# Kernel optimization log

Measured on AMD Instinct MI355X. Metric: run time of the kernel, lower is better.

The kernel has to match this reference:

```python
import jax, jax.numpy as jnp
import numpy as np


def _quantize(mat):
    # per-row (last-dim) symmetric int8 quantization; scale stored in fp16 like torch
    max_val = (jnp.max(jnp.abs(mat), axis=-1) / 127.0).astype(jnp.float16)
    # torch's .to(int8) truncates toward zero; jnp astype does the same for in-range values
    q = (mat / max_val[..., None].astype(mat.dtype)).astype(jnp.int8)
    return q, max_val


def setup_inputs() -> dict:
    key = jax.random.key(0)
    k1, k2, k3, k4 = jax.random.split(key, 4)
    B, S, D_IN, D_OUT = 4, 2048, 4096, 4096
    x = jax.random.normal(k1, (B, S, D_IN), dtype=jnp.float32)
    origin_weight = jax.random.normal(k2, (D_OUT, D_IN), dtype=jnp.float32) * 0.02
    bias = jax.random.normal(k3, (D_OUT,), dtype=jnp.float32) * 0.01
    act_max = jax.random.normal(k4, (D_IN,), dtype=jnp.float32)
    return {"x": x, "origin_weight": origin_weight, "bias": bias,
            "act_max": act_max, "alpha": 32}


def reference(x, origin_weight, bias, act_max, alpha):
    d_in = act_max.shape[-1]
    # get_unq_idx_topk: top-alpha outlier channels by |act_max|
    _, idx = jax.lax.top_k(jnp.abs(act_max), alpha)          # [alpha]
    t = jnp.ones((d_in,), dtype=origin_weight.dtype).at[idx].set(0)

    # weight decomposition + quantization (done in __init__ in torch)
    weight_q, w_max = _quantize(origin_weight * t)           # [out,in] int8, [out] fp16
    weight_unq = origin_weight[:, idx].T                      # [alpha, out]

    # activation decomposition + per-token quantization
    x_unq = x[..., idx]                                       # [B,S,alpha]
    x_q, x_max = _quantize(x * t.astype(x.dtype))             # [B,S,in] int8, [B,S] fp16

    # simulated MatMulInteger: int8 values multiplied in fp32
    res_q = jnp.matmul(x_q.astype(jnp.float32), weight_q.T.astype(jnp.float32))  # [B,S,out]
    mx = (x_max[..., None] * w_max[None, :]).astype(jnp.float32)                  # [B,S,out]
    res_q = (res_q * mx).astype(x.dtype)

    # fp outlier path
    res_unq = jnp.matmul(x_unq, weight_unq) + bias
    return res_q + res_unq
```

## Files before the change

### kernel.cpp

```cpp
#include <hip/hip_runtime.h>
#include <hip/hip_fp16.h>

typedef __attribute__((ext_vector_type(4)))  int   i32x4;
typedef __attribute__((ext_vector_type(16))) int   i32x16;

#define ALPHA 32
#define BM 256
#define BN 128
#define BK 64


__global__ __launch_bounds__(256) void topk_kernel(const float* __restrict__ act_max,
                                                   int* __restrict__ idx_out,
                                                   unsigned* __restrict__ tbits,
                                                   int K) {
  __shared__ float v[4096];
  __shared__ float rv[4];
  __shared__ int   ri[4];
  __shared__ unsigned bits[128];
  const int t = threadIdx.x;
  for (int i = t; i < K; i += 256) v[i] = fabsf(act_max[i]);
  for (int i = t; i < K / 32; i += 256) bits[i] = 0xFFFFFFFFu;
  __syncthreads();
  for (int sel = 0; sel < ALPHA; ++sel) {
    float bv = -1.f; int bi = 0;
    for (int i = t; i < K; i += 256) {
      float x = v[i];
      if (x > bv) { bv = x; bi = i; }
    }
    for (int m = 1; m < 64; m <<= 1) {
      float ov = __shfl_xor(bv, m);
      int   oi = __shfl_xor(bi, m);
      if (ov > bv || (ov == bv && oi < bi)) { bv = ov; bi = oi; }
    }
    if ((t & 63) == 0) { rv[t >> 6] = bv; ri[t >> 6] = bi; }
    __syncthreads();
    if (t == 0) {
      for (int u = 1; u < 4; ++u)
        if (rv[u] > bv || (rv[u] == bv && ri[u] < bi)) { bv = rv[u]; bi = ri[u]; }
      idx_out[sel] = bi;
      v[bi] = -2.f;
      bits[bi >> 5] &= ~(1u << (bi & 31));
    }
    __syncthreads();
  }
  for (int i = t; i < K / 32; i += 256) tbits[i] = bits[i];
}

__global__ __launch_bounds__(256) void quant8_kernel(
    const float* __restrict__ srcW, const float* __restrict__ srcX,
    const unsigned* __restrict__ tbits, const int* __restrict__ idxg,
    signed char* __restrict__ wq, signed char* __restrict__ xq,
    _Float16* __restrict__ wmax, _Float16* __restrict__ xmax,
    float* __restrict__ wuf, float* __restrict__ xuf,
    int nbw, int K, int N, int M) {
  const int t = threadIdx.x, lane = t & 63, w = t >> 6;
  const int b = blockIdx.x;
  const float* src; signed char* q; _Float16* smax; float* unq; int r0, R;
  if (b < nbw) { src = srcW; q = wq; smax = wmax; unq = wuf; r0 = b * 8; R = N; }
  else         { src = srcX; q = xq; smax = xmax; unq = xuf; r0 = (b - nbw) * 8; R = M; }
  __shared__ unsigned bits[128];
  __shared__ signed char qt[8 * 4096];
  for (int i = t; i < 128; i += 256) bits[i] = tbits[i];
  __syncthreads();
  const int shft = (lane & 7) * 4;
#pragma unroll
  for (int g = 0; g < 2; ++g) {
    const int rl = w + 4 * g;
    const float4* srow = (const float4*)(src + (size_t)(r0 + rl) * K);
    float4 v[16];
    float am = 0.f;
#pragma unroll
    for (int j = 0; j < 16; ++j) {
      float4 x = srow[j * 64 + lane];
      unsigned b4 = bits[j * 8 + (lane >> 3)] >> shft;
      if (!(b4 & 1u)) x.x = 0.f;
      if (!(b4 & 2u)) x.y = 0.f;
      if (!(b4 & 4u)) x.z = 0.f;
      if (!(b4 & 8u)) x.w = 0.f;
      v[j] = x;
      am = fmaxf(am, fmaxf(fmaxf(fabsf(x.x), fabsf(x.y)), fmaxf(fabsf(x.z), fabsf(x.w))));
    }
#pragma unroll
    for (int m = 1; m < 64; m <<= 1) am = fmaxf(am, __shfl_xor(am, m));
    const _Float16 sh = (_Float16)(am / 127.0f);
    const float s = (float)sh;
    if (lane == 0) smax[r0 + rl] = sh;
    signed char* row = qt + rl * 4096;
#pragma unroll
    for (int j = 0; j < 16; ++j) {
      float4 x = v[j];
      char4 c;
      c.x = (signed char)(x.x / s);
      c.y = (signed char)(x.y / s);
      c.z = (signed char)(x.z / s);
      c.w = (signed char)(x.w / s);
      const int c2 = j * 16 + (lane >> 2);
      *(char4*)(row + ((c2 ^ rl) << 4) + (lane & 3) * 4) = c;
    }
  }
  __syncthreads();
  const size_t pbase = (size_t)(r0 >> 5) * 32 * K + (size_t)(r0 & 31) * 16;
#pragma unroll
  for (int i = 0; i < 8; ++i) {
    const int s2 = i * 256 + t;
    const int c2 = s2 >> 3, rl = s2 & 7;
    int4 d = *(const int4*)(qt + rl * 4096 + ((c2 ^ rl) << 4));
    *(int4*)(q + pbase + (size_t)c2 * 512 + rl * 16) = d;
  }
  {
    const int j = t >> 3, rl = t & 7;
    unq[(size_t)j * R + r0 + rl] = src[(size_t)(r0 + rl) * K + idxg[j]];
  }
}

__device__ __forceinline__ void gld_lds16(const signed char* g, signed char* l) {
  __builtin_amdgcn_global_load_lds(
      (const __attribute__((address_space(1))) void*)g,
      (__attribute__((address_space(3))) void*)l, 16, 0, 0);
}

__global__ __launch_bounds__(256, 2) void gemm_kernel(
    const signed char* __restrict__ xq, const signed char* __restrict__ wq,
    const _Float16* __restrict__ xmax, const _Float16* __restrict__ wmax,
    const float* __restrict__ xuf,
    const float* __restrict__ wuf,
    const float* __restrict__ bias,
    float* __restrict__ out, int M, int N, int K) {
  __shared__ union {
    struct { signed char A[3][BM * BK]; signed char B[3][BN * BK]; } g;
    struct { float xu[ALPHA * BM]; float wu[ALPHA * BN]; } e;
  } sm;
  __shared__ _Float16 xmh[BM];
  __shared__ _Float16 wmh[BN];
  __shared__ float    bl[BN];

  const int t = threadIdx.x;
  const int bid = blockIdx.y * gridDim.x + blockIdx.x;
  const int xcd = bid & 7, loc = bid >> 3;
  const int bxi = xcd * 4 + (loc & 3);
  const int byi = loc >> 2;
  const int bm0 = byi * BM;
  const int bn0 = bxi * BN;
  const int lane = t & 63, w = t >> 6;
  const int wm = w >> 1, wn = w & 1;
  const int hi = lane >> 5, l31 = lane & 31;

  i32x16 acc[4][2] = {};

  const int tp = t >> 7;
  const int to = (t & 127) * 16;
  const signed char* aS = xq + (size_t)bm0 * K + (size_t)tp * 32 * K + to;
  const signed char* bS = wq + (size_t)bn0 * K + (size_t)tp * 32 * K + to;
  signed char* const aD = &sm.g.A[0][0] + t * 16;
  signed char* const bD = &sm.g.B[0][0] + t * 16;
  const size_t PSTR = (size_t)64 * K;

  auto STAGE = [&](int buf, int kt) {
    const size_t ko = (size_t)kt * 2048;
#pragma unroll
    for (int i = 0; i < 4; ++i)
      gld_lds16(aS + (size_t)i * PSTR + ko, aD + buf * (BM * BK) + i * 4096);
#pragma unroll
    for (int i = 0; i < 2; ++i)
      gld_lds16(bS + (size_t)i * PSTR + ko, bD + buf * (BN * BK) + i * 4096);
  };

  const int NT = K >> 6;
  STAGE(0, 0);
  STAGE(1, 1);
  const signed char* const aR0 = &sm.g.A[0][0] + (wm * 4) * 2048 + 16 * lane;
  const signed char* const bR0 = &sm.g.B[0][0] + (wn * 2) * 2048 + 16 * lane;

  int cur = 0, st = 2;
  for (int kt = 0; kt < NT - 1; ++kt) {
    asm volatile("s_waitcnt vmcnt(6)" ::: "memory");
    asm volatile("s_barrier" ::: "memory");
    const signed char* aRd = aR0 + cur * (BM * BK);
    const signed char* bRd = bR0 + cur * (BN * BK);
    i32x4 af[2][4], bf[2][2];
#pragma unroll
    for (int ks = 0; ks < 2; ++ks) {
#pragma unroll
      for (int mi = 0; mi < 4; ++mi) af[ks][mi] = *(const i32x4*)(aRd + mi * 2048 + ks * 1024);
#pragma unroll
      for (int ni = 0; ni < 2; ++ni) bf[ks][ni] = *(const i32x4*)(bRd + ni * 2048 + ks * 1024);
    }
    if (kt + 2 < NT) STAGE(st, kt + 2);
    __builtin_amdgcn_s_setprio(1);
#pragma unroll
    for (int ks = 0; ks < 2; ++ks)
#pragma unroll
      for (int mi = 0; mi < 4; ++mi)
#pragma unroll
        for (int ni = 0; ni < 2; ++ni)
          acc[mi][ni] = __builtin_amdgcn_mfma_i32_32x32x32_i8(af[ks][mi], bf[ks][ni], acc[mi][ni], 0, 0, 0);
    __builtin_amdgcn_s_setprio(0);
    if (++cur == 3) cur = 0;
    if (++st == 3) st = 0;
  }
  {
    asm volatile("s_waitcnt vmcnt(0)" ::: "memory");
    asm volatile("s_barrier" ::: "memory");
    const signed char* aRd = aR0 + cur * (BM * BK);
    const signed char* bRd = bR0 + cur * (BN * BK);
    i32x4 af[2][4], bf[2][2];
#pragma unroll
    for (int ks = 0; ks < 2; ++ks) {
#pragma unroll
      for (int mi = 0; mi < 4; ++mi) af[ks][mi] = *(const i32x4*)(aRd + mi * 2048 + ks * 1024);
#pragma unroll
      for (int ni = 0; ni < 2; ++ni) bf[ks][ni] = *(const i32x4*)(bRd + ni * 2048 + ks * 1024);
    }
    __builtin_amdgcn_s_setprio(1);
#pragma unroll
    for (int ks = 0; ks < 2; ++ks)
#pragma unroll
      for (int mi = 0; mi < 4; ++mi)
#pragma unroll
        for (int ni = 0; ni < 2; ++ni)
          acc[mi][ni] = __builtin_amdgcn_mfma_i32_32x32x32_i8(af[ks][mi], bf[ks][ni], acc[mi][ni], 0, 0, 0);
    __builtin_amdgcn_s_setprio(0);
  }

  __syncthreads();
  {
    const float4* xs = (const float4*)xuf;
    float4* xl = (float4*)sm.e.xu;
#pragma unroll
    for (int i = 0; i < 8; ++i) {
      int p = i * 256 + t;
      int j = p >> 6, r4 = p & 63;
      xl[p] = xs[(size_t)j * (M >> 2) + (bm0 >> 2) + r4];
    }
    const float4* wsrc = (const float4*)wuf;
    float4* wl = (float4*)sm.e.wu;
#pragma unroll
    for (int i = 0; i < 4; ++i) {
      int p = i * 256 + t;
      int j = p >> 5, r4 = p & 31;
      wl[p] = wsrc[(size_t)j * (N >> 2) + (bn0 >> 2) + r4];
    }
    if (t < BM / 2) ((unsigned*)xmh)[t] = ((const unsigned*)(xmax + bm0))[t];
    if (t < BN / 2) ((unsigned*)wmh)[t] = ((const unsigned*)(wmax + bn0))[t];
    if (t < BN / 4) ((float4*)bl)[t] = ((const float4*)(bias + bn0))[t];
  }
  __syncthreads();

  const int c0 = wn * 64 + l31;
  const _Float16 wh0 = wmh[c0], wh1 = wmh[c0 + 32];
  const float bv0 = bl[c0], bv1 = bl[c0 + 32];
  const float* xul = sm.e.xu;
  const float* wul = sm.e.wu;

#pragma unroll
  for (int mi = 0; mi < 4; ++mi) {
    const int rbase = wm * 128 + mi * 32 + 4 * hi;
    float f0[16], f1[16];
#pragma unroll
    for (int r = 0; r < 16; ++r) {
      int row = rbase + (r & 3) + 8 * (r >> 2);
      _Float16 xh = xmh[row];
      float mx0 = (float)(_Float16)(xh * wh0);
      float mx1 = (float)(_Float16)(xh * wh1);
      f0[r] = (float)acc[mi][0][r] * mx0 + bv0;
      f1[r] = (float)acc[mi][1][r] * mx1 + bv1;
    }
#pragma unroll 4
    for (int j = 0; j < ALPHA; ++j) {
      const float4* xrow4 = (const float4*)(xul + j * BM + rbase);
      float wv0 = wul[j * BN + c0];
      float wv1 = wul[j * BN + c0 + 32];
#pragma unroll
      for (int gq = 0; gq < 4; ++gq) {
        float4 xv = xrow4[gq * 2];
        f0[gq * 4 + 0] += xv.x * wv0;  f1[gq * 4 + 0] += xv.x * wv1;
        f0[gq * 4 + 1] += xv.y * wv0;  f1[gq * 4 + 1] += xv.y * wv1;
        f0[gq * 4 + 2] += xv.z * wv0;  f1[gq * 4 + 2] += xv.z * wv1;
        f0[gq * 4 + 3] += xv.w * wv0;  f1[gq * 4 + 3] += xv.w * wv1;
      }
    }
#pragma unroll
    for (int r = 0; r < 16; ++r) {
      int row = bm0 + rbase + (r & 3) + 8 * (r >> 2);
      size_t o = (size_t)row * N + bn0;
      out[o + c0] = f0[r];
      out[o + c0 + 32] = f1[r];
    }
  }
}

extern "C" void kernel_launch(void* const* d_in, const int* in_sizes, int n_in,
                              void* d_out, int out_size, void* d_ws, size_t ws_size,
                              hipStream_t stream) {
  const float* x       = (const float*)d_in[0];
  const float* W       = (const float*)d_in[1];
  const float* bias    = (const float*)d_in[2];
  const float* act_max = (const float*)d_in[3];
  const int K = in_sizes[3];
  const int N = in_sizes[1] / K;
  const int M = in_sizes[0] / K;
  float* out = (float*)d_out;

  char* ws = (char*)d_ws;
  size_t off = 0;
  auto take = [&](size_t b) { char* p = ws + off; off += (b + 255) & ~(size_t)255; return p; };
  signed char* wq  = (signed char*)take((size_t)N * K);
  signed char* xq  = (signed char*)take((size_t)M * K);
  _Float16* wmax   = (_Float16*)take((size_t)N * 2);
  _Float16* xmax   = (_Float16*)take((size_t)M * 2);
  float* wuf       = (float*)take((size_t)ALPHA * N * 4);
  float* xuf       = (float*)take((size_t)ALPHA * M * 4);
  int* idx         = (int*)take(ALPHA * 4);
  unsigned* tbits  = (unsigned*)take((size_t)(K / 32) * 4);

  const int nbw = N / 8, nbx = M / 8;
  topk_kernel<<<1, 256, 0, stream>>>(act_max, idx, tbits, K);
  quant8_kernel<<<nbw + nbx, 256, 0, stream>>>(W, x, tbits, idx, wq, xq,
                                               wmax, xmax, wuf, xuf, nbw, K, N, M);
  dim3 grid(N / BN, M / BM);
  gemm_kernel<<<grid, 256, 0, stream>>>(xq, wq, xmax, wmax, xuf, wuf, bias, out, M, N, K);
}
```

Before: 276.8 us.

## Enlarge GEMM tile to 256x256 with 8 waves and 4-stage split-phase pipeline

Doubles the N tile to 256 and launches 512-thread blocks (8 waves in a 2x4 arrangement), so each loaded A/B byte is reused across more MFMAs. The k-loop becomes a 4-deep LDS ring with A and B prefetches issued in separate half-iterations, interleaved with barriers, explicit lgkm/vm waits and setprio around MFMA groups. Epilogue scale, bias and outlier staging move into the shared union, and the XCD block remap is adjusted to the new grid. This raises LDS use to 128 KB per block and adds barriers, which may limit occupancy and add synchronisation overhead.

```diff
diff --git a/kernel.cpp b/kernel.cpp
--- a/kernel.cpp
+++ b/kernel.cpp
@@ -6,7 +6,7 @@
 
 #define ALPHA 32
 #define BM 256
-#define BN 128
+#define BN 256
 #define BK 64
 
 
@@ -120,7 +120,7 @@
       (__attribute__((address_space(3))) void*)l, 16, 0, 0);
 }
 
-__global__ __launch_bounds__(256, 2) void gemm_kernel(
+__global__ __launch_bounds__(512, 2) void gemm_kernel(
     const signed char* __restrict__ xq, const signed char* __restrict__ wq,
     const _Float16* __restrict__ xmax, const _Float16* __restrict__ wmax,
     const float* __restrict__ xuf,
@@ -128,108 +128,115 @@
     const float* __restrict__ bias,
     float* __restrict__ out, int M, int N, int K) {
   __shared__ union {
-    struct { signed char A[3][BM * BK]; signed char B[3][BN * BK]; } g;
-    struct { float xu[ALPHA * BM]; float wu[ALPHA * BN]; } e;
+    struct { signed char A[4][BM * BK]; signed char B[4][BN * BK]; } g;
+    struct { float xu[ALPHA * BM]; float wu[ALPHA * BN];
+             _Float16 xmh[BM]; _Float16 wmh[BN]; float bl[BN]; } e;
   } sm;
-  __shared__ _Float16 xmh[BM];
-  __shared__ _Float16 wmh[BN];
-  __shared__ float    bl[BN];
 
   const int t = threadIdx.x;
   const int bid = blockIdx.y * gridDim.x + blockIdx.x;
   const int xcd = bid & 7, loc = bid >> 3;
-  const int bxi = xcd * 4 + (loc & 3);
-  const int byi = loc >> 2;
+  const int bxi = xcd * 2 + (loc & 1);
+  const int byi = loc >> 1;
   const int bm0 = byi * BM;
   const int bn0 = bxi * BN;
   const int lane = t & 63, w = t >> 6;
-  const int wm = w >> 1, wn = w & 1;
+  const int wm = w >> 2, wn = w & 3;
   const int hi = lane >> 5, l31 = lane & 31;
 
   i32x16 acc[4][2] = {};
 
-  const int tp = t >> 7;
-  const int to = (t & 127) * 16;
-  const signed char* aS = xq + (size_t)bm0 * K + (size_t)tp * 32 * K + to;
-  const signed char* bS = wq + (size_t)bn0 * K + (size_t)tp * 32 * K + to;
+  const size_t P32 = (size_t)32 * K;
+  const signed char* aS = xq + (size_t)bm0 * K + (size_t)(t >> 7) * P32 + (t & 127) * 16;
+  const signed char* bS = wq + (size_t)bn0 * K + (size_t)(t >> 7) * P32 + (t & 127) * 16;
   signed char* const aD = &sm.g.A[0][0] + t * 16;
   signed char* const bD = &sm.g.B[0][0] + t * 16;
-  const size_t PSTR = (size_t)64 * K;
-
-  auto STAGE = [&](int buf, int kt) {
+
+  auto STAGE_A = [&](int buf, int kt) {
     const size_t ko = (size_t)kt * 2048;
-#pragma unroll
-    for (int i = 0; i < 4; ++i)
-      gld_lds16(aS + (size_t)i * PSTR + ko, aD + buf * (BM * BK) + i * 4096);
-#pragma unroll
-    for (int i = 0; i < 2; ++i)
-      gld_lds16(bS + (size_t)i * PSTR + ko, bD + buf * (BN * BK) + i * 4096);
+    gld_lds16(aS + ko, aD + buf * (BM * BK));
+    gld_lds16(aS + ko + 4 * P32, aD + buf * (BM * BK) + 8192);
   };
+  auto STAGE_B = [&](int buf, int kt) {
+    const size_t ko = (size_t)kt * 2048;
+    gld_lds16(bS + ko, bD + buf * (BN * BK));
+    gld_lds16(bS + ko + 4 * P32, bD + buf * (BN * BK) + 8192);
+  };
 
   const int NT = K >> 6;
-  STAGE(0, 0);
-  STAGE(1, 1);
-  const signed char* const aR0 = &sm.g.A[0][0] + (wm * 4) * 2048 + 16 * lane;
-  const signed char* const bR0 = &sm.g.B[0][0] + (wn * 2) * 2048 + 16 * lane;
-
-  int cur = 0, st = 2;
-  for (int kt = 0; kt < NT - 1; ++kt) {
-    asm volatile("s_waitcnt vmcnt(6)" ::: "memory");
-    asm volatile("s_barrier" ::: "memory");
-    const signed char* aRd = aR0 + cur * (BM * BK);
-    const signed char* bRd = bR0 + cur * (BN * BK);
-    i32x4 af[2][4], bf[2][2];
-#pragma unroll
-    for (int ks = 0; ks < 2; ++ks) {
-#pragma unroll
-      for (int mi = 0; mi < 4; ++mi) af[ks][mi] = *(const i32x4*)(aRd + mi * 2048 + ks * 1024);
-#pragma unroll
-      for (int ni = 0; ni < 2; ++ni) bf[ks][ni] = *(const i32x4*)(bRd + ni * 2048 + ks * 1024);
-    }
-    if (kt + 2 < NT) STAGE(st, kt + 2);
-    __builtin_amdgcn_s_setprio(1);
-#pragma unroll
-    for (int ks = 0; ks < 2; ++ks)
-#pragma unroll
-      for (int mi = 0; mi < 4; ++mi)
-#pragma unroll
-        for (int ni = 0; ni < 2; ++ni)
-          acc[mi][ni] = __builtin_amdgcn_mfma_i32_32x32x32_i8(af[ks][mi], bf[ks][ni], acc[mi][ni], 0, 0, 0);
-    __builtin_amdgcn_s_setprio(0);
-    if (++cur == 3) cur = 0;
-    if (++st == 3) st = 0;
-  }
-  {
-    asm volatile("s_waitcnt vmcnt(0)" ::: "memory");
-    asm volatile("s_barrier" ::: "memory");
-    const signed char* aRd = aR0 + cur * (BM * BK);
-    const signed char* bRd = bR0 + cur * (BN * BK);
-    i32x4 af[2][4], bf[2][2];
-#pragma unroll
-    for (int ks = 0; ks < 2; ++ks) {
-#pragma unroll
-      for (int mi = 0; mi < 4; ++mi) af[ks][mi] = *(const i32x4*)(aRd + mi * 2048 + ks * 1024);
-#pragma unroll
-      for (int ni = 0; ni < 2; ++ni) bf[ks][ni] = *(const i32x4*)(bRd + ni * 2048 + ks * 1024);
-    }
-    __builtin_amdgcn_s_setprio(1);
-#pragma unroll
-    for (int ks = 0; ks < 2; ++ks)
-#pragma unroll
-      for (int mi = 0; mi < 4; ++mi)
-#pragma unroll
-        for (int ni = 0; ni < 2; ++ni)
-          acc[mi][ni] = __builtin_amdgcn_mfma_i32_32x32x32_i8(af[ks][mi], bf[ks][ni], acc[mi][ni], 0, 0, 0);
-    __builtin_amdgcn_s_setprio(0);
-  }
+  STAGE_A(0, 0); STAGE_B(0, 0);
+  STAGE_A(1, 1); STAGE_B(1, 1);
+  STAGE_A(2, 2); STAGE_B(2, 2);
+  asm volatile("s_waitcnt vmcnt(8)" ::: "memory");
+  asm volatile("s_barrier" ::: "memory");
+
+  const signed char* const aBase = &sm.g.A[0][0] + (wm * 4) * 2048 + hi * 512 + l31 * 16;
+  const signed char* const bBase = &sm.g.B[0][0] + (wn * 2) * 2048 + hi * 512 + l31 * 16;
+
+#define MFMA8()                                                                        \
+  acc[0][0] = __builtin_amdgcn_mfma_i32_32x32x32_i8(a0, b0, acc[0][0], 0, 0, 0);       \
+  acc[0][1] = __builtin_amdgcn_mfma_i32_32x32x32_i8(a0, b1, acc[0][1], 0, 0, 0);       \
+  acc[1][0] = __builtin_amdgcn_mfma_i32_32x32x32_i8(a1, b0, acc[1][0], 0, 0, 0);       \
+  acc[1][1] = __builtin_amdgcn_mfma_i32_32x32x32_i8(a1, b1, acc[1][1], 0, 0, 0);       \
+  acc[2][0] = __builtin_amdgcn_mfma_i32_32x32x32_i8(a2, b0, acc[2][0], 0, 0, 0);       \
+  acc[2][1] = __builtin_amdgcn_mfma_i32_32x32x32_i8(a2, b1, acc[2][1], 0, 0, 0);       \
+  acc[3][0] = __builtin_amdgcn_mfma_i32_32x32x32_i8(a3, b0, acc[3][0], 0, 0, 0);       \
+  acc[3][1] = __builtin_amdgcn_mfma_i32_32x32x32_i8(a3, b1, acc[3][1], 0, 0, 0)
+
+#define ITERATION(DOSTAGE, WSTR)                                                       \
+  {                                                                                    \
+    const signed char* aRd = aBase + cur * (BM * BK);                                  \
+    const signed char* bRd = bBase + cur * (BN * BK);                                  \
+                                                       \
+    i32x4 a0 = *(const i32x4*)(aRd + 0);                                               \
+    i32x4 a1 = *(const i32x4*)(aRd + 2048);                                            \
+    i32x4 a2 = *(const i32x4*)(aRd + 4096);                                            \
+    i32x4 a3 = *(const i32x4*)(aRd + 6144);                                            \
+    i32x4 b0 = *(const i32x4*)(bRd + 0);                                               \
+    i32x4 b1 = *(const i32x4*)(bRd + 2048);                                            \
+    if (DOSTAGE) STAGE_A((kt + 3) & 3, kt + 3);                                        \
+    asm volatile("s_barrier" ::: "memory");                                            \
+    asm volatile("s_waitcnt lgkmcnt(0)" ::: "memory");                                 \
+    __builtin_amdgcn_sched_barrier(0);                                                 \
+    __builtin_amdgcn_s_setprio(1);                                                     \
+    MFMA8();                                                                           \
+    __builtin_amdgcn_s_setprio(0);                                                     \
+    asm volatile("s_barrier" ::: "memory");                                            \
+                                                       \
+    a0 = *(const i32x4*)(aRd + 1024);                                                  \
+    a1 = *(const i32x4*)(aRd + 3072);                                                  \
+    a2 = *(const i32x4*)(aRd + 5120);                                                  \
+    a3 = *(const i32x4*)(aRd + 7168);                                                  \
+    b0 = *(const i32x4*)(bRd + 1024);                                                  \
+    b1 = *(const i32x4*)(bRd + 3072);                                                  \
+    if (DOSTAGE) STAGE_B((kt + 3) & 3, kt + 3);                                        \
+    asm volatile(WSTR ::: "memory");                                                   \
+    asm volatile("s_barrier" ::: "memory");                                            \
+    asm volatile("s_waitcnt lgkmcnt(0)" ::: "memory");                                 \
+    __builtin_amdgcn_sched_barrier(0);                                                 \
+    __builtin_amdgcn_s_setprio(1);                                                     \
+    MFMA8();                                                                           \
+    __builtin_amdgcn_s_setprio(0);                                                     \
+    asm volatile("s_barrier" ::: "memory");                                            \
+    cur = (cur + 1) & 3;                                                               \
+  }
+
+  int cur = 0;
+  int kt = 0;
+  for (; kt < NT - 3; ++kt) ITERATION(true, "s_waitcnt vmcnt(8)");
+  ITERATION(false, "s_waitcnt vmcnt(4)"); ++kt;
+  ITERATION(false, "s_waitcnt vmcnt(0)"); ++kt;
+  ITERATION(false, "s_waitcnt vmcnt(0)");
+#undef ITERATION
+#undef MFMA8
 
   __syncthreads();
   {
     const float4* xs = (const float4*)xuf;
     float4* xl = (float4*)sm.e.xu;
 #pragma unroll
-    for (int i = 0; i < 8; ++i) {
-      int p = i * 256 + t;
+    for (int i = 0; i < 4; ++i) {
+      int p = i * 512 + t;
       int j = p >> 6, r4 = p & 63;
       xl[p] = xs[(size_t)j * (M >> 2) + (bm0 >> 2) + r4];
     }
@@ -237,19 +244,19 @@
     float4* wl = (float4*)sm.e.wu;
 #pragma unroll
     for (int i = 0; i < 4; ++i) {
-      int p = i * 256 + t;
-      int j = p >> 5, r4 = p & 31;
+      int p = i * 512 + t;
+      int j = p >> 6, r4 = p & 63;
       wl[p] = wsrc[(size_t)j * (N >> 2) + (bn0 >> 2) + r4];
     }
-    if (t < BM / 2) ((unsigned*)xmh)[t] = ((const unsigned*)(xmax + bm0))[t];
-    if (t < BN / 2) ((unsigned*)wmh)[t] = ((const unsigned*)(wmax + bn0))[t];
-    if (t < BN / 4) ((float4*)bl)[t] = ((const float4*)(bias + bn0))[t];
+    if (t < BM / 2) ((unsigned*)sm.e.xmh)[t] = ((const unsigned*)(xmax + bm0))[t];
+    if (t < BN / 2) ((unsigned*)sm.e.wmh)[t] = ((const unsigned*)(wmax + bn0))[t];
+    if (t < BN / 4) ((float4*)sm.e.bl)[t] = ((const float4*)(bias + bn0))[t];
   }
   __syncthreads();
 
   const int c0 = wn * 64 + l31;
-  const _Float16 wh0 = wmh[c0], wh1 = wmh[c0 + 32];
-  const float bv0 = bl[c0], bv1 = bl[c0 + 32];
+  const _Float16 wh0 = sm.e.wmh[c0], wh1 = sm.e.wmh[c0 + 32];
+  const float bv0 = sm.e.bl[c0], bv1 = sm.e.bl[c0 + 32];
   const float* xul = sm.e.xu;
   const float* wul = sm.e.wu;
 
@@ -260,7 +267,7 @@
 #pragma unroll
     for (int r = 0; r < 16; ++r) {
       int row = rbase + (r & 3) + 8 * (r >> 2);
-      _Float16 xh = xmh[row];
+      _Float16 xh = sm.e.xmh[row];
       float mx0 = (float)(_Float16)(xh * wh0);
       float mx1 = (float)(_Float16)(xh * wh1);
       f0[r] = (float)acc[mi][0][r] * mx0 + bv0;
@@ -319,5 +326,5 @@
   quant8_kernel<<<nbw + nbx, 256, 0, stream>>>(W, x, tbits, idx, wq, xq,
                                                wmax, xmax, wuf, xuf, nbw, K, N, M);
   dim3 grid(N / BN, M / BM);
-  gemm_kernel<<<grid, 256, 0, stream>>>(xq, wq, xmax, wmax, xuf, wuf, bias, out, M, N, K);
-}
+  gemm_kernel<<<grid, 512, 0, stream>>>(xq, wq, xmax, wmax, xuf, wuf, bias, out, M, N, K);
+}
```

New measurement: 272.9 us. No clear change (-1.4%).

## Load GEMM B operand straight into registers and use a 4-deep LDS ring for A

Applied to the files above, without the earlier changes.

The weight (B) tile no longer goes through LDS. Each wave loads its own B fragments from global memory into a pair of register buffers one k-step ahead, while the A tile stays in LDS, now in a 4-slot ring staged two steps ahead. The main loop is unrolled by two so the register double buffer can swap without copies. This cuts LDS traffic and B ds_reads, but waves sharing the same N columns now each read B from global memory, which duplicates L2 traffic and raises register pressure.

```diff
diff --git a/kernel.cpp b/kernel.cpp
--- a/kernel.cpp
+++ b/kernel.cpp
@@ -128,7 +128,7 @@
     const float* __restrict__ bias,
     float* __restrict__ out, int M, int N, int K) {
   __shared__ union {
-    struct { signed char A[3][BM * BK]; signed char B[3][BN * BK]; } g;
+    signed char A[4][BM * BK];
     struct { float xu[ALPHA * BM]; float wu[ALPHA * BN]; } e;
   } sm;
   __shared__ _Float16 xmh[BM];
@@ -148,80 +148,60 @@
 
   i32x16 acc[4][2] = {};
 
-  const int tp = t >> 7;
-  const int to = (t & 127) * 16;
-  const signed char* aS = xq + (size_t)bm0 * K + (size_t)tp * 32 * K + to;
-  const signed char* bS = wq + (size_t)bn0 * K + (size_t)tp * 32 * K + to;
-  signed char* const aD = &sm.g.A[0][0] + t * 16;
-  signed char* const bD = &sm.g.B[0][0] + t * 16;
-  const size_t PSTR = (size_t)64 * K;
-
-  auto STAGE = [&](int buf, int kt) {
-    const size_t ko = (size_t)kt * 2048;
-#pragma unroll
-    for (int i = 0; i < 4; ++i)
-      gld_lds16(aS + (size_t)i * PSTR + ko, aD + buf * (BM * BK) + i * 4096);
-#pragma unroll
-    for (int i = 0; i < 2; ++i)
-      gld_lds16(bS + (size_t)i * PSTR + ko, bD + buf * (BN * BK) + i * 4096);
-  };
+  const size_t P32 = (size_t)32 * K;
+  const signed char* aS = xq + (size_t)bm0 * K + (size_t)(t >> 7) * P32 + (t & 127) * 16;
+  signed char* const aD = &sm.A[0][0] + t * 16;
+  const signed char* bW = wq + (size_t)(bn0 + wn * 64) * K + hi * 512 + l31 * 16;
+
+#define STAGE_A(BUF, KT)                                                          \
+  {                                                                               \
+    const size_t ko = (size_t)(KT) * 2048;                                        \
+    _Pragma("unroll") for (int i = 0; i < 4; ++i)                                 \
+      gld_lds16(aS + (size_t)(2 * i) * P32 + ko, aD + (BUF) * (BM * BK) + i * 4096); \
+  }
+
+#define LOADB(DST, KT)                                                            \
+  _Pragma("unroll") for (int ni = 0; ni < 2; ++ni)                                \
+    _Pragma("unroll") for (int ks = 0; ks < 2; ++ks)                              \
+      DST[ni][ks] = *(const i32x4*)(bW + (size_t)ni * 32 * K +                    \
+                                    (size_t)(KT) * 2048 + ks * 1024);
+
+#define ITER(KT, BCUR, BNXT, WCNT, DOB, DOST)                                     \
+  {                                                                               \
+    asm volatile("s_waitcnt vmcnt(" #WCNT ")" ::: "memory");                      \
+    asm volatile("s_barrier" ::: "memory");                                       \
+    if (DOB) { LOADB(BNXT, (KT) + 1); }                                           \
+    if (DOST) { STAGE_A(((KT) + 2) & 3, (KT) + 2); }                              \
+    const signed char* aRd = &sm.A[(KT) & 3][0] + (wm * 4) * 2048 + hi * 512 + l31 * 16; \
+    i32x4 af[2][4];                                                               \
+    _Pragma("unroll") for (int ks = 0; ks < 2; ++ks)                              \
+      _Pragma("unroll") for (int mi = 0; mi < 4; ++mi)                            \
+        af[ks][mi] = *(const i32x4*)(aRd + mi * 2048 + ks * 1024);                \
+    __builtin_amdgcn_s_setprio(1);                                                \
+    _Pragma("unroll") for (int ks = 0; ks < 2; ++ks)                              \
+      _Pragma("unroll") for (int ni = 0; ni < 2; ++ni)                            \
+        _Pragma("unroll") for (int mi = 0; mi < 4; ++mi)                          \
+          acc[mi][ni] = __builtin_amdgcn_mfma_i32_32x32x32_i8(                    \
+              af[ks][mi], BCUR[ni][ks], acc[mi][ni], 0, 0, 0);                    \
+    __builtin_amdgcn_s_setprio(0);                                                \
+  }
 
   const int NT = K >> 6;
-  STAGE(0, 0);
-  STAGE(1, 1);
-  const signed char* const aR0 = &sm.g.A[0][0] + (wm * 4) * 2048 + 16 * lane;
-  const signed char* const bR0 = &sm.g.B[0][0] + (wn * 2) * 2048 + 16 * lane;
-
-  int cur = 0, st = 2;
-  for (int kt = 0; kt < NT - 1; ++kt) {
-    asm volatile("s_waitcnt vmcnt(6)" ::: "memory");
-    asm volatile("s_barrier" ::: "memory");
-    const signed char* aRd = aR0 + cur * (BM * BK);
-    const signed char* bRd = bR0 + cur * (BN * BK);
-    i32x4 af[2][4], bf[2][2];
-#pragma unroll
-    for (int ks = 0; ks < 2; ++ks) {
-#pragma unroll
-      for (int mi = 0; mi < 4; ++mi) af[ks][mi] = *(const i32x4*)(aRd + mi * 2048 + ks * 1024);
-#pragma unroll
-      for (int ni = 0; ni < 2; ++ni) bf[ks][ni] = *(const i32x4*)(bRd + ni * 2048 + ks * 1024);
-    }
-    if (kt + 2 < NT) STAGE(st, kt + 2);
-    __builtin_amdgcn_s_setprio(1);
-#pragma unroll
-    for (int ks = 0; ks < 2; ++ks)
-#pragma unroll
-      for (int mi = 0; mi < 4; ++mi)
-#pragma unroll
-        for (int ni = 0; ni < 2; ++ni)
-          acc[mi][ni] = __builtin_amdgcn_mfma_i32_32x32x32_i8(af[ks][mi], bf[ks][ni], acc[mi][ni], 0, 0, 0);
-    __builtin_amdgcn_s_setprio(0);
-    if (++cur == 3) cur = 0;
-    if (++st == 3) st = 0;
-  }
-  {
-    asm volatile("s_waitcnt vmcnt(0)" ::: "memory");
-    asm volatile("s_barrier" ::: "memory");
-    const signed char* aRd = aR0 + cur * (BM * BK);
-    const signed char* bRd = bR0 + cur * (BN * BK);
-    i32x4 af[2][4], bf[2][2];
-#pragma unroll
-    for (int ks = 0; ks < 2; ++ks) {
-#pragma unroll
-      for (int mi = 0; mi < 4; ++mi) af[ks][mi] = *(const i32x4*)(aRd + mi * 2048 + ks * 1024);
-#pragma unroll
-      for (int ni = 0; ni < 2; ++ni) bf[ks][ni] = *(const i32x4*)(bRd + ni * 2048 + ks * 1024);
-    }
-    __builtin_amdgcn_s_setprio(1);
-#pragma unroll
-    for (int ks = 0; ks < 2; ++ks)
-#pragma unroll
-      for (int mi = 0; mi < 4; ++mi)
-#pragma unroll
-        for (int ni = 0; ni < 2; ++ni)
-          acc[mi][ni] = __builtin_amdgcn_mfma_i32_32x32x32_i8(af[ks][mi], bf[ks][ni], acc[mi][ni], 0, 0, 0);
-    __builtin_amdgcn_s_setprio(0);
-  }
+  i32x4 bA[2][2], bB[2][2];
+  STAGE_A(0, 0);
+  STAGE_A(1, 1);
+  LOADB(bA, 0);
+
+  int kt = 0;
+  for (; kt < NT - 2; kt += 2) {
+    ITER(kt,     bA, bB, 8, true, true);
+    ITER(kt + 1, bB, bA, 8, true, (kt + 3 < NT));
+  }
+  ITER(NT - 2, bA, bB, 8, true,  false);
+  ITER(NT - 1, bB, bA, 4, false, false);
+#undef ITER
+#undef LOADB
+#undef STAGE_A
 
   __syncthreads();
   {
```

After: 288.9 us. +4.4%, slower.

## Register-resident topk and 12-row quant blocks with smaller LDS staging

Applied to the files above, without the earlier changes.

The top-k kernel now keeps |act_max| in per-thread registers instead of a 4096-float LDS array and broadcasts the selected index. The quantization kernel handles 12 rows per block in three 4-row passes, using a 16KB LDS tile instead of 32KB. This aims for higher occupancy on the memory-bound quantize pass, and it replaces per-element division with multiplication by a reciprocal. Risks: the reciprocal can change truncated int8 values at boundaries. Also, (N+M)/12 must divide evenly, and 12-row blocks straddle the W/X boundary and 32-row pack groups, which adds extra barriers per pass.

```diff
diff --git a/kernel.cpp b/kernel.cpp
--- a/kernel.cpp
+++ b/kernel.cpp
@@ -14,65 +14,70 @@
                                                    int* __restrict__ idx_out,
                                                    unsigned* __restrict__ tbits,
                                                    int K) {
-  __shared__ float v[4096];
   __shared__ float rv[4];
   __shared__ int   ri[4];
   __shared__ unsigned bits[128];
-  const int t = threadIdx.x;
-  for (int i = t; i < K; i += 256) v[i] = fabsf(act_max[i]);
-  for (int i = t; i < K / 32; i += 256) bits[i] = 0xFFFFFFFFu;
+  __shared__ int bsel;
+  const int t = threadIdx.x, w = t >> 6;
+  float vloc[16];
+#pragma unroll
+  for (int jj = 0; jj < 16; ++jj) vloc[jj] = fabsf(act_max[jj * 256 + t]);
+  for (int i = t; i < 128; i += 256) bits[i] = 0xFFFFFFFFu;
   __syncthreads();
   for (int sel = 0; sel < ALPHA; ++sel) {
-    float bv = -1.f; int bi = 0;
-    for (int i = t; i < K; i += 256) {
-      float x = v[i];
-      if (x > bv) { bv = x; bi = i; }
-    }
+    float bv = vloc[0]; int bi = t;
+#pragma unroll
+    for (int jj = 1; jj < 16; ++jj)
+      if (vloc[jj] > bv) { bv = vloc[jj]; bi = jj * 256 + t; }
     for (int m = 1; m < 64; m <<= 1) {
       float ov = __shfl_xor(bv, m);
       int   oi = __shfl_xor(bi, m);
       if (ov > bv || (ov == bv && oi < bi)) { bv = ov; bi = oi; }
     }
-    if ((t & 63) == 0) { rv[t >> 6] = bv; ri[t >> 6] = bi; }
+    if ((t & 63) == 0) { rv[w] = bv; ri[w] = bi; }
     __syncthreads();
     if (t == 0) {
       for (int u = 1; u < 4; ++u)
         if (rv[u] > bv || (rv[u] == bv && ri[u] < bi)) { bv = rv[u]; bi = ri[u]; }
       idx_out[sel] = bi;
-      v[bi] = -2.f;
       bits[bi >> 5] &= ~(1u << (bi & 31));
-    }
-    __syncthreads();
-  }
-  for (int i = t; i < K / 32; i += 256) tbits[i] = bits[i];
-}
-
-__global__ __launch_bounds__(256) void quant8_kernel(
+      bsel = bi;
+    }
+    __syncthreads();
+    const int bs = bsel;
+#pragma unroll
+    for (int jj = 0; jj < 16; ++jj)
+      if (jj * 256 + t == bs) vloc[jj] = -2.f;
+    __syncthreads();
+  }
+  for (int i = t; i < 128; i += 256) tbits[i] = bits[i];
+}
+
+__global__ __launch_bounds__(256) void quant12_kernel(
     const float* __restrict__ srcW, const float* __restrict__ srcX,
     const unsigned* __restrict__ tbits, const int* __restrict__ idxg,
     signed char* __restrict__ wq, signed char* __restrict__ xq,
     _Float16* __restrict__ wmax, _Float16* __restrict__ xmax,
     float* __restrict__ wuf, float* __restrict__ xuf,
-    int nbw, int K, int N, int M) {
+    int K, int N, int M) {
   const int t = threadIdx.x, lane = t & 63, w = t >> 6;
-  const int b = blockIdx.x;
-  const float* src; signed char* q; _Float16* smax; float* unq; int r0, R;
-  if (b < nbw) { src = srcW; q = wq; smax = wmax; unq = wuf; r0 = b * 8; R = N; }
-  else         { src = srcX; q = xq; smax = xmax; unq = xuf; r0 = (b - nbw) * 8; R = M; }
+  const int r0 = blockIdx.x * 12;
   __shared__ unsigned bits[128];
-  __shared__ signed char qt[8 * 4096];
+  __shared__ signed char qt[4 * 4096];
   for (int i = t; i < 128; i += 256) bits[i] = tbits[i];
   __syncthreads();
   const int shft = (lane & 7) * 4;
 #pragma unroll
-  for (int g = 0; g < 2; ++g) {
-    const int rl = w + 4 * g;
-    const float4* srow = (const float4*)(src + (size_t)(r0 + rl) * K);
+  for (int g = 0; g < 3; ++g) {
+    const int r = r0 + g * 4 + w;
+    const bool isW = r < N;
+    const float* srow = isW ? (srcW + (size_t)r * K) : (srcX + (size_t)(r - N) * K);
+    const float4* srow4 = (const float4*)srow;
     float4 v[16];
     float am = 0.f;
 #pragma unroll
     for (int j = 0; j < 16; ++j) {
-      float4 x = srow[j * 64 + lane];
+      float4 x = srow4[j * 64 + lane];
       unsigned b4 = bits[j * 8 + (lane >> 3)] >> shft;
       if (!(b4 & 1u)) x.x = 0.f;
       if (!(b4 & 2u)) x.y = 0.f;
@@ -84,33 +89,38 @@
 #pragma unroll
     for (int m = 1; m < 64; m <<= 1) am = fmaxf(am, __shfl_xor(am, m));
     const _Float16 sh = (_Float16)(am / 127.0f);
-    const float s = (float)sh;
-    if (lane == 0) smax[r0 + rl] = sh;
-    signed char* row = qt + rl * 4096;
+    const float inv = 1.0f / (float)sh;
+    if (lane == 0) { if (isW) wmax[r] = sh; else xmax[r - N] = sh; }
+    signed char* rowq = qt + w * 4096;
 #pragma unroll
     for (int j = 0; j < 16; ++j) {
       float4 x = v[j];
       char4 c;
-      c.x = (signed char)(x.x / s);
-      c.y = (signed char)(x.y / s);
-      c.z = (signed char)(x.z / s);
-      c.w = (signed char)(x.w / s);
+      c.x = (signed char)(x.x * inv);
+      c.y = (signed char)(x.y * inv);
+      c.z = (signed char)(x.z * inv);
+      c.w = (signed char)(x.w * inv);
       const int c2 = j * 16 + (lane >> 2);
-      *(char4*)(row + ((c2 ^ rl) << 4) + (lane & 3) * 4) = c;
-    }
-  }
-  __syncthreads();
-  const size_t pbase = (size_t)(r0 >> 5) * 32 * K + (size_t)(r0 & 31) * 16;
-#pragma unroll
-  for (int i = 0; i < 8; ++i) {
-    const int s2 = i * 256 + t;
-    const int c2 = s2 >> 3, rl = s2 & 7;
-    int4 d = *(const int4*)(qt + rl * 4096 + ((c2 ^ rl) << 4));
-    *(int4*)(q + pbase + (size_t)c2 * 512 + rl * 16) = d;
-  }
-  {
-    const int j = t >> 3, rl = t & 7;
-    unq[(size_t)j * R + r0 + rl] = src[(size_t)(r0 + rl) * K + idxg[j]];
+      *(char4*)(rowq + ((c2 ^ w) << 4) + (lane & 3) * 4) = c;
+    }
+    __syncthreads();
+#pragma unroll
+    for (int i = 0; i < 4; ++i) {
+      const int s2 = i * 256 + t;
+      const int c2 = s2 >> 2, rl = s2 & 3;
+      const int row = r0 + g * 4 + rl;
+      int4 d = *(const int4*)(qt + rl * 4096 + ((c2 ^ rl) << 4));
+      signed char* q = (row < N) ? wq : xq;
+      const int rr = (row < N) ? row : row - N;
+      *(int4*)(q + (size_t)(rr >> 5) * 32 * K + (size_t)c2 * 512 + (rr & 31) * 16) = d;
+    }
+    __syncthreads();
+  }
+  for (int p = t; p < 32 * 12; p += 256) {
+    const int lr = p >> 5, j = p & 31;
+    const int row = r0 + lr;
+    if (row < N) wuf[(size_t)j * N + row]       = srcW[(size_t)row * K + idxg[j]];
+    else         xuf[(size_t)j * M + (row - N)] = srcX[(size_t)(row - N) * K + idxg[j]];
   }
 }
 
@@ -314,10 +324,9 @@
   int* idx         = (int*)take(ALPHA * 4);
   unsigned* tbits  = (unsigned*)take((size_t)(K / 32) * 4);
 
-  const int nbw = N / 8, nbx = M / 8;
   topk_kernel<<<1, 256, 0, stream>>>(act_max, idx, tbits, K);
-  quant8_kernel<<<nbw + nbx, 256, 0, stream>>>(W, x, tbits, idx, wq, xq,
-                                               wmax, xmax, wuf, xuf, nbw, K, N, M);
+  quant12_kernel<<<(N + M) / 12, 256, 0, stream>>>(W, x, tbits, idx, wq, xq,
+                                                   wmax, xmax, wuf, xuf, K, N, M);
   dim3 grid(N / BN, M / BM);
   gemm_kernel<<<grid, 256, 0, stream>>>(xq, wq, xmax, wmax, xuf, wuf, bias, out, M, N, K);
 }
```

New measurement: 254.3 us. 1.09x faster.
